# Kernel tuning notes

Hardware: AMD Instinct MI355X
Metric: run time of the kernel (lower is better)

Reference implementation:

```python
import jax, jax.numpy as jnp
import numpy as np
from jax import lax

HEADS = 4
NEG_SLOPE = 0.2


def _layernorm(x, g, b, eps=1e-5):
    m = x.mean(-1, keepdims=True)
    v = ((x - m) ** 2).mean(-1, keepdims=True)
    return (x - m) * lax.rsqrt(v + eps) * g + b


def setup_inputs() -> dict:
    key = jax.random.key(0)
    ks = jax.random.split(key, 10)
    B, N, T, H, E, ED, K = 1, 1000, 32, 128, 16000, 16, 3
    s_h = 1.0 / np.sqrt(H)
    s_e = 1.0 / np.sqrt(ED)
    return {
        "x": jax.random.normal(ks[0], (B, N, T, H), jnp.float32),
        "edge_index": jax.random.randint(ks[1], (2, E), 0, N, dtype=jnp.int32),
        "edge_attr": jax.random.normal(ks[2], (E, ED), jnp.float32),
        "conv_w": jax.random.normal(ks[3], (H, H, K), jnp.float32) * (1.0 / np.sqrt(H * K)),
        "conv_b": jnp.zeros((H,), jnp.float32),
        "ln1_g": jnp.ones((H,), jnp.float32),
        "ln1_b": jnp.zeros((H,), jnp.float32),
        "Wl": jax.random.normal(ks[4], (H, H), jnp.float32) * s_h,
        "Wr": jax.random.normal(ks[5], (H, H), jnp.float32) * s_h,
        "We": jax.random.normal(ks[6], (ED, H), jnp.float32) * s_e,
        "att": jax.random.normal(ks[7], (HEADS, H // HEADS), jnp.float32) * s_h,
        "gat_b": jnp.zeros((H,), jnp.float32),
        "ln2_g": jnp.ones((H,), jnp.float32),
        "ln2_b": jnp.zeros((H,), jnp.float32),
    }


def reference(x, edge_index, edge_attr, conv_w, conv_b, ln1_g, ln1_b,
              Wl, Wr, We, att, gat_b, ln2_g, ln2_b):
    B, N, T, H = x.shape
    K = HEADS
    D = H // K
    E = edge_attr.shape[0]

    # ---- temporal sub-block: per-node Conv1d over time ('same' padding) ----
    xt = x.reshape(B * N, T, H).transpose(0, 2, 1)            # [BN, H, T]
    y = lax.conv_general_dilated(xt, conv_w, (1,), 'SAME',
                                 dimension_numbers=('NCH', 'OIH', 'NCH'))
    y = y + conv_b[None, :, None]
    y = y.transpose(0, 2, 1).reshape(B, N, T, H)
    x = _layernorm(x + y, ln1_g, ln1_b)

    # ---- spatial sub-block: GATv2 at every timestep (mega-batch of G graphs) ----
    G = B * T
    xs = x.transpose(0, 2, 1, 3).reshape(G, N, H)             # [G, N, H]

    # add self-loops, fill_value='mean' (mean of incoming edge attrs per node)
    dst0 = edge_index[1]
    cnt = jax.ops.segment_sum(jnp.ones((E,), edge_attr.dtype), dst0, num_segments=N)
    loop_attr = jax.ops.segment_sum(edge_attr, dst0, num_segments=N) / jnp.maximum(cnt, 1.0)[:, None]
    ea = jnp.concatenate([edge_attr, loop_attr], axis=0)       # [E+N, ED]
    loops = jnp.arange(N, dtype=edge_index.dtype)
    src = jnp.concatenate([edge_index[0], loops])
    dst = jnp.concatenate([edge_index[1], loops])

    gl = jnp.einsum('gnh,hkd->gnkd', xs, Wl.reshape(H, K, D))  # source transform
    gr = jnp.einsum('gnh,hkd->gnkd', xs, Wr.reshape(H, K, D))  # target transform
    ee = jnp.einsum('ef,fkd->ekd', ea, We.reshape(-1, K, D))   # edge transform

    e_src = jnp.swapaxes(gl[:, src], 0, 1)                     # [E', G, K, D]
    e_dst = jnp.swapaxes(gr[:, dst], 0, 1)                     # [E', G, K, D]
    s = jax.nn.leaky_relu(e_src + e_dst + ee[:, None], NEG_SLOPE)
    logits = jnp.einsum('egkd,kd->egk', s, att)                # [E', G, K]

    # scatter-softmax over incoming edges per target node (self-loops => non-empty)
    mx = jax.ops.segment_max(logits, dst, num_segments=N)[dst]
    ex = jnp.exp(logits - mx)
    den = jax.ops.segment_sum(ex, dst, num_segments=N)[dst]
    alpha = ex / den

    aggr = jax.ops.segment_sum(e_src * alpha[..., None], dst, num_segments=N)  # [N, G, K, D]
    out = jnp.swapaxes(aggr, 0, 1).reshape(G, N, H) + gat_b

    out = out.reshape(B, T, N, H).transpose(0, 2, 1, 3)        # back to (B, N, T, H)
    return _layernorm(x + out, ln2_g, ln2_b)
```

## Files before the change

kernel.cpp:

```cpp
#include <hip/hip_runtime.h>
#include <math.h>

#define N_NODES 1000
#define T_STEPS 32
#define H_DIM   128
#define E_EDGES 16000
#define ED_DIM  16
#define G_GRAPHS 32
#define EP_EDGES (E_EDGES + N_NODES)
#define NEG_SLOPE 0.2f
#define LN_EPS 1e-5f

typedef __attribute__((ext_vector_type(8))) short bf16x8;
typedef __attribute__((ext_vector_type(16))) float f32x16;
typedef __attribute__((ext_vector_type(4))) float f32x4;
typedef unsigned short u16;

__device__ inline short f2bf(float f) {
    unsigned u = __float_as_uint(f);
    u = (u + 0x7FFFu + ((u >> 16) & 1u)) >> 16;
    return (short)u;
}
__device__ inline float bf2f(u16 u) { return __uint_as_float(((unsigned)u) << 16); }
__device__ inline float bflo(unsigned u) { return __uint_as_float(u << 16); }
__device__ inline float bfhi(unsigned u) { return __uint_as_float(u & 0xFFFF0000u); }

__global__ void k_pack(const float* __restrict__ conv_w, const float* __restrict__ Wl,
                       const float* __restrict__ Wr, short* __restrict__ wc,
                       short* __restrict__ wg) {
    int i = blockIdx.x * 256 + threadIdx.x;
    if (i < 4 * 24 * 64 * 8) {
        int r = i & 7, lane = (i >> 3) & 63;
        int t = i >> 9;
        int kstep = t % 24, ct = t / 24;
        int k = kstep >> 3, hs = kstep & 7;
        int hi = hs * 16 + ((lane >> 5) << 3) + r;
        int o = ct * 32 + (lane & 31);
        wc[i] = f2bf(conv_w[(o * H_DIM + hi) * 3 + k]);
    } else {
        int j = i - 4 * 24 * 64 * 8;
        if (j >= 8 * 8 * 64 * 8) return;
        int r = j & 7, lane = (j >> 3) & 63;
        int ks = (j >> 9) & 7, ct = j >> 12;
        int hi = ks * 16 + ((lane >> 5) << 3) + r;
        int o = ct * 32 + (lane & 31);
        wg[j] = f2bf(o < H_DIM ? Wl[hi * H_DIM + o] : Wr[hi * H_DIM + o - H_DIM]);
    }
}

__global__ __launch_bounds__(1024) void k_countscan(const int* __restrict__ dst,
                                                    int* __restrict__ cnt, int* __restrict__ cnt2,
                                                    int* __restrict__ offs) {
    __shared__ int sm[1024];
    int t = threadIdx.x;
    sm[t] = 0;
    __syncthreads();
    for (int e = t; e < E_EDGES; e += 1024) atomicAdd(&sm[dst[e]], 1);
    __syncthreads();
    int v = (t < N_NODES) ? sm[t] : 0;
    if (t < N_NODES) { cnt[t] = v; cnt2[t] = 0; }
    __syncthreads();
    sm[t] = v;
    for (int s = 1; s < 1024; s <<= 1) {
        __syncthreads();
        int a = (t >= s) ? sm[t - s] : 0;
        __syncthreads();
        sm[t] += a;
    }
    __syncthreads();
    if (t < N_NODES) offs[t + 1] = sm[t];
    if (t == 0) offs[0] = 0;
}

__global__ void k_place(const int* __restrict__ dst, const int* __restrict__ offs,
                        int* __restrict__ cnt2, int* __restrict__ csr) {
    int e = blockIdx.x * 256 + threadIdx.x;
    if (e >= E_EDGES) return;
    int d = dst[e];
    int slot = atomicAdd(&cnt2[d], 1);
    csr[offs[d] + slot] = e;
}

__global__ __launch_bounds__(64) void k_sortla(
    const float* __restrict__ edge_attr, int* __restrict__ csr,
    const int* __restrict__ offs, const int* __restrict__ cnt,
    float* __restrict__ loop_attr) {
    __shared__ int buf[128];
    int n = blockIdx.x;
    int lane = threadIdx.x;
    int off = offs[n], deg = cnt[n];

    if (deg <= 64) {
        int v = (lane < deg) ? csr[off + lane] : 0x7FFFFFFF;
        int rank = 0;
#pragma unroll
        for (int j = 0; j < 64; ++j) {
            int vj = __shfl(v, j);
            rank += (vj < v) ? 1 : 0;
        }
        if (lane < deg) buf[rank] = v;
    } else {
        for (int i = lane; i < deg && i < 128; i += 64) buf[i] = csr[off + i];
        __syncthreads();
        if (lane == 0) {
            int dd = deg < 128 ? deg : 128;
            for (int i = 1; i < dd; ++i) {
                int key = buf[i], j = i - 1;
                while (j >= 0 && buf[j] > key) { buf[j + 1] = buf[j]; --j; }
                buf[j + 1] = key;
            }
        }
    }
    __syncthreads();
    if (lane < deg) csr[off + lane] = buf[lane];

    int q = lane >> 4, f = lane & 15;
    float a = 0.f;
    for (int i = q; i < deg; i += 4) a += edge_attr[buf[i] * ED_DIM + f];
    a += __shfl_xor(a, 16);
    a += __shfl_xor(a, 32);
    if (lane < 16) loop_attr[n * ED_DIM + lane] = a / fmaxf((float)deg, 1.0f);
}

__global__ void k_ee(const float* __restrict__ edge_attr, const float* __restrict__ loop_attr,
                     const float* __restrict__ We, u16* __restrict__ ee) {
    int e = blockIdx.x * 2 + (threadIdx.x >> 7);
    int h = threadIdx.x & 127;
    if (e >= EP_EDGES) return;
    const float* ea = (e < E_EDGES) ? &edge_attr[e * ED_DIM]
                                    : &loop_attr[(e - E_EDGES) * ED_DIM];
    float acc = 0.f;
#pragma unroll
    for (int f = 0; f < ED_DIM; ++f) acc += ea[f] * We[f * H_DIM + h];
    ee[e * H_DIM + h] = (u16)f2bf(acc);
}

__global__ __launch_bounds__(256) void k_temporal(
    const float* __restrict__ x, const short* __restrict__ wc, const short* __restrict__ wg,
    const float* __restrict__ conv_b, const float* __restrict__ ln1_g,
    const float* __restrict__ ln1_b, float* __restrict__ x1,
    u16* __restrict__ gl, u16* __restrict__ gr) {
    __shared__ __align__(16) short xb[34 * 136];
    __shared__ float yb[32 * 132];
    int n = blockIdx.x;
    int tid = threadIdx.x;
    int w = tid >> 6, lane = tid & 63;
    int arow = lane & 31;
    int aks = (lane >> 5) << 3;

    {
        const float4* xs4 = (const float4*)(x + (size_t)n * T_STEPS * H_DIM);
        for (int i4 = tid; i4 < T_STEPS * H_DIM / 4; i4 += 256) {
            float4 v = xs4[i4];
            int t = i4 >> 5, h = (i4 * 4) & 127;
            uint2 pp;
            pp.x = (unsigned)(unsigned short)f2bf(v.x) | ((unsigned)(unsigned short)f2bf(v.y) << 16);
            pp.y = (unsigned)(unsigned short)f2bf(v.z) | ((unsigned)(unsigned short)f2bf(v.w) << 16);
            *(uint2*)&xb[(t + 1) * 136 + h] = pp;
        }
        if (tid < 68) {
            ((unsigned*)xb)[tid] = 0u;
            ((unsigned*)(xb + 33 * 136))[tid] = 0u;
        }
    }
    __syncthreads();

    f32x16 acc = {};
    for (int kk = 0; kk < 3; ++kk) {
#pragma unroll
        for (int hs = 0; hs < 8; ++hs) {
            int kstep = kk * 8 + hs;
            bf16x8 a = *(const bf16x8*)&xb[(arow + kk) * 136 + hs * 16 + aks];
            bf16x8 b = *(const bf16x8*)&wc[((w * 24 + kstep) * 64 + lane) * 8];
            acc = __builtin_amdgcn_mfma_f32_32x32x16_bf16(a, b, acc, 0, 0, 0);
        }
    }
    {
        int oc = w * 32 + (lane & 31);
        float cb = conv_b[oc];
#pragma unroll
        for (int r = 0; r < 16; ++r) {
            int t = (r & 3) + 8 * (r >> 2) + 4 * (lane >> 5);
            yb[t * 132 + oc] = acc[r] + cb;
        }
    }
    __syncthreads();

    for (int t = w; t < T_STEPS; t += 4) {
        float r0 = x[((size_t)n * T_STEPS + t) * H_DIM + lane] + yb[t * 132 + lane];
        float r1 = x[((size_t)n * T_STEPS + t) * H_DIM + lane + 64] + yb[t * 132 + lane + 64];
        float s = r0 + r1, s2 = r0 * r0 + r1 * r1;
#pragma unroll
        for (int mm = 1; mm < 64; mm <<= 1) {
            s += __shfl_xor(s, mm);
            s2 += __shfl_xor(s2, mm);
        }
        float mean = s * (1.f / 128.f);
        float var = s2 * (1.f / 128.f) - mean * mean;
        float rs = rsqrtf(var + LN_EPS);
        float o0 = (r0 - mean) * rs * ln1_g[lane] + ln1_b[lane];
        float o1 = (r1 - mean) * rs * ln1_g[lane + 64] + ln1_b[lane + 64];
        x1[((size_t)n * T_STEPS + t) * H_DIM + lane] = o0;
        x1[((size_t)n * T_STEPS + t) * H_DIM + lane + 64] = o1;
        xb[t * 136 + lane] = f2bf(o0);
        xb[t * 136 + lane + 64] = f2bf(o1);
    }
    __syncthreads();

    f32x16 cl = {}, cr = {};
#pragma unroll
    for (int ks = 0; ks < 8; ++ks) {
        bf16x8 a = *(const bf16x8*)&xb[arow * 136 + ks * 16 + aks];
        bf16x8 b0 = *(const bf16x8*)&wg[(((2 * w) * 8 + ks) * 64 + lane) * 8];
        bf16x8 b1 = *(const bf16x8*)&wg[(((2 * w + 1) * 8 + ks) * 64 + lane) * 8];
        cl = __builtin_amdgcn_mfma_f32_32x32x16_bf16(a, b0, cl, 0, 0, 0);
        cr = __builtin_amdgcn_mfma_f32_32x32x16_bf16(a, b1, cr, 0, 0, 0);
    }
    {
        int o0 = 64 * w + (lane & 31);
        u16* d = (w < 2) ? gl : gr;
        int oo0 = (w < 2) ? o0 : o0 - 128;
        int oo1 = oo0 + 32;
#pragma unroll
        for (int r = 0; r < 16; ++r) {
            int t = (r & 3) + 8 * (r >> 2) + 4 * (lane >> 5);
            d[((size_t)t * N_NODES + n) * H_DIM + oo0] = (u16)f2bf(cl[r]);
            d[((size_t)t * N_NODES + n) * H_DIM + oo1] = (u16)f2bf(cr[r]);
        }
    }
}

__global__ __launch_bounds__(128) void k_gat(
    const u16* __restrict__ gl, const u16* __restrict__ gr, const u16* __restrict__ ee,
    const int* __restrict__ src_arr, const int* __restrict__ csr,
    const int* __restrict__ offs, const int* __restrict__ cnt,
    const float* __restrict__ att, const float* __restrict__ gat_b,
    const float* __restrict__ x1, const float* __restrict__ ln2_g,
    const float* __restrict__ ln2_b, float* __restrict__ out) {
    int bid = blockIdx.x;
    int q = bid & 3;
    int n = bid >> 2;
    int tid = threadIdx.x;
    int gs = tid >> 4;
    int r = tid & 15;
    int h0 = ((r >> 2) << 5) + ((r & 3) << 3);
    int g = q + 4 * gs;

    __shared__ int es[64], ss[64];
    int off = offs[n], deg = cnt[n];
    int tot = deg + 1;

    float av[8], grv[8];
    {
        float4 a0 = *(const float4*)&att[h0];
        float4 a1 = *(const float4*)&att[h0 + 4];
        av[0] = a0.x; av[1] = a0.y; av[2] = a0.z; av[3] = a0.w;
        av[4] = a1.x; av[5] = a1.y; av[6] = a1.z; av[7] = a1.w;
        uint4 g4 = *(const uint4*)&gr[((size_t)g * N_NODES + n) * H_DIM + h0];
        grv[0] = bflo(g4.x); grv[1] = bfhi(g4.x); grv[2] = bflo(g4.y); grv[3] = bfhi(g4.y);
        grv[4] = bflo(g4.z); grv[5] = bfhi(g4.z); grv[6] = bflo(g4.w); grv[7] = bfhi(g4.w);
    }
    const u16* glg = gl + (size_t)g * N_NODES * H_DIM + h0;
    const u16* eeh = ee + h0;

    float m = -INFINITY, l = 0.f;
    float ac[8] = {0.f, 0.f, 0.f, 0.f, 0.f, 0.f, 0.f, 0.f};

    for (int base = 0; base < tot; base += 64) {
        int c = min(64, tot - base);
        __syncthreads();
        if (tid < c) {
            int i = base + tid;
            int e = (i < deg) ? csr[off + i] : (E_EDGES + n);
            es[tid] = e;
            ss[tid] = (i < deg) ? src_arr[e] : n;
        }
        __syncthreads();
        uint4 gv4 = *(const uint4*)&glg[(size_t)ss[0] * H_DIM];
        uint4 ev4 = *(const uint4*)&eeh[(size_t)es[0] * H_DIM];
        for (int i = 0; i < c; ++i) {
            uint4 gc = gv4, ec = ev4;
            if (i + 1 < c) {
                gv4 = *(const uint4*)&glg[(size_t)ss[i + 1] * H_DIM];
                ev4 = *(const uint4*)&eeh[(size_t)es[i + 1] * H_DIM];
            }
            float gv[8];
            gv[0] = bflo(gc.x); gv[1] = bfhi(gc.x); gv[2] = bflo(gc.y); gv[3] = bfhi(gc.y);
            gv[4] = bflo(gc.z); gv[5] = bfhi(gc.z); gv[6] = bflo(gc.w); gv[7] = bfhi(gc.w);
            float ev[8];
            ev[0] = bflo(ec.x); ev[1] = bfhi(ec.x); ev[2] = bflo(ec.y); ev[3] = bfhi(ec.y);
            ev[4] = bflo(ec.z); ev[5] = bfhi(ec.z); ev[6] = bflo(ec.w); ev[7] = bfhi(ec.w);
            float p = 0.f;
#pragma unroll
            for (int j = 0; j < 8; ++j) {
                float sf = gv[j] + grv[j] + ev[j];
                sf = fmaxf(sf, NEG_SLOPE * sf);
                p = fmaf(sf, av[j], p);
            }
            p += __shfl_xor(p, 1);
            p += __shfl_xor(p, 2);
            bool grow = p > m + 8.f;
            if (__any(grow)) {
                float mn = fmaxf(m, p);
                float sc = __expf(m - mn);
                float wq = __expf(p - mn);
                l = l * sc + wq;
#pragma unroll
                for (int j = 0; j < 8; ++j) ac[j] = ac[j] * sc + wq * gv[j];
                m = mn;
            } else {
                float wq = __expf(p - m);
                l += wq;
#pragma unroll
                for (int j = 0; j < 8; ++j) ac[j] += wq * gv[j];
            }
        }
    }

    float linv = 1.0f / l;
    size_t ob = ((size_t)n * T_STEPS + g) * H_DIM + h0;
    float4 x0 = *(const float4*)&x1[ob];
    float4 x1v = *(const float4*)&x1[ob + 4];
    float4 gb0 = *(const float4*)&gat_b[h0];
    float4 gb1 = *(const float4*)&gat_b[h0 + 4];
    float rv[8];
    rv[0] = x0.x + ac[0] * linv + gb0.x;
    rv[1] = x0.y + ac[1] * linv + gb0.y;
    rv[2] = x0.z + ac[2] * linv + gb0.z;
    rv[3] = x0.w + ac[3] * linv + gb0.w;
    rv[4] = x1v.x + ac[4] * linv + gb1.x;
    rv[5] = x1v.y + ac[5] * linv + gb1.y;
    rv[6] = x1v.z + ac[6] * linv + gb1.z;
    rv[7] = x1v.w + ac[7] * linv + gb1.w;
    float s1 = 0.f, s2v = 0.f;
#pragma unroll
    for (int j = 0; j < 8; ++j) { s1 += rv[j]; s2v += rv[j] * rv[j]; }
#pragma unroll
    for (int mm = 1; mm < 16; mm <<= 1) {
        s1 += __shfl_xor(s1, mm);
        s2v += __shfl_xor(s2v, mm);
    }
    float mean = s1 * (1.f / 128.f);
    float var = s2v * (1.f / 128.f) - mean * mean;
    float rs = rsqrtf(var + LN_EPS);
    float4 g20 = *(const float4*)&ln2_g[h0];
    float4 g21 = *(const float4*)&ln2_g[h0 + 4];
    float4 b20 = *(const float4*)&ln2_b[h0];
    float4 b21 = *(const float4*)&ln2_b[h0 + 4];
    f32x4 o0, o1;
    o0.x = (rv[0] - mean) * rs * g20.x + b20.x;
    o0.y = (rv[1] - mean) * rs * g20.y + b20.y;
    o0.z = (rv[2] - mean) * rs * g20.z + b20.z;
    o0.w = (rv[3] - mean) * rs * g20.w + b20.w;
    o1.x = (rv[4] - mean) * rs * g21.x + b21.x;
    o1.y = (rv[5] - mean) * rs * g21.y + b21.y;
    o1.z = (rv[6] - mean) * rs * g21.z + b21.z;
    o1.w = (rv[7] - mean) * rs * g21.w + b21.w;
    __builtin_nontemporal_store(o0, (f32x4*)&out[ob]);
    __builtin_nontemporal_store(o1, (f32x4*)&out[ob + 4]);
}

extern "C" void kernel_launch(void* const* d_in, const int* in_sizes, int n_in,
                              void* d_out, int out_size, void* d_ws, size_t ws_size,
                              hipStream_t stream) {
    const float* x         = (const float*)d_in[0];
    const int*   ei        = (const int*)d_in[1];
    const float* edge_attr = (const float*)d_in[2];
    const float* conv_w    = (const float*)d_in[3];
    const float* conv_b    = (const float*)d_in[4];
    const float* ln1_g     = (const float*)d_in[5];
    const float* ln1_b     = (const float*)d_in[6];
    const float* Wl        = (const float*)d_in[7];
    const float* Wr        = (const float*)d_in[8];
    const float* We        = (const float*)d_in[9];
    const float* att       = (const float*)d_in[10];
    const float* gat_b     = (const float*)d_in[11];
    const float* ln2_g     = (const float*)d_in[12];
    const float* ln2_b     = (const float*)d_in[13];
    float* out = (float*)d_out;

    const int* src = ei;
    const int* dst = ei + E_EDGES;

    float* x1   = (float*)d_ws;
    u16*   glb  = (u16*)(x1 + 4096000);
    u16*   grb  = glb + 4096000;
    u16*   eeb  = grb + 4096000;
    float* la   = (float*)(eeb + 2176000);
    int* ibase  = (int*)(la + 16000);
    int* cnt    = ibase;
    int* cnt2   = ibase + 1000;
    int* offs   = ibase + 2000;
    int* csr    = ibase + 3001;
    short* wc   = (short*)(ibase + 19008);
    short* wg   = wc + 49152;

    k_pack<<<320, 256, 0, stream>>>(conv_w, Wl, Wr, wc, wg);
    k_countscan<<<1, 1024, 0, stream>>>(dst, cnt, cnt2, offs);
    k_place<<<(E_EDGES + 255) / 256, 256, 0, stream>>>(dst, offs, cnt2, csr);
    k_sortla<<<N_NODES, 64, 0, stream>>>(edge_attr, csr, offs, cnt, la);
    k_ee<<<(EP_EDGES + 1) / 2, 256, 0, stream>>>(edge_attr, la, We, eeb);
    k_temporal<<<N_NODES, 256, 0, stream>>>(x, wc, wg, conv_b, ln1_g, ln1_b, x1, glb, grb);
    k_gat<<<4 * N_NODES, 128, 0, stream>>>(glb, grb, eeb, src, csr, offs, cnt,
                                           att, gat_b, x1, ln2_g, ln2_b, out);
}
```

Baseline: 88.94 us.

## Merge preprocessing kernels and simplify GAT online softmax inner loop

Five small preprocessing launches become two. Weight packing, degree counting, the scan and CSR placement share one launch, and CSR sorting, self-loop attribute means and the edge transform share another. This cuts launch overhead and the serial gaps between tiny kernels. In the GAT kernel, edge-feature loads become nontemporal and the branchy lazy-rescale softmax becomes an unconditional rescale, trading extra exps per edge for less divergence and shorter control flow.

```diff
diff --git a/kernel.cpp b/kernel.cpp
--- a/kernel.cpp
+++ b/kernel.cpp
@@ -14,6 +14,7 @@
 typedef __attribute__((ext_vector_type(8))) short bf16x8;
 typedef __attribute__((ext_vector_type(16))) float f32x16;
 typedef __attribute__((ext_vector_type(4))) float f32x4;
+typedef __attribute__((ext_vector_type(4))) unsigned u32x4;
 typedef unsigned short u16;
 
 __device__ inline short f2bf(float f) {
@@ -21,46 +22,44 @@
     u = (u + 0x7FFFu + ((u >> 16) & 1u)) >> 16;
     return (short)u;
 }
-__device__ inline float bf2f(u16 u) { return __uint_as_float(((unsigned)u) << 16); }
 __device__ inline float bflo(unsigned u) { return __uint_as_float(u << 16); }
 __device__ inline float bfhi(unsigned u) { return __uint_as_float(u & 0xFFFF0000u); }
 
-__global__ void k_pack(const float* __restrict__ conv_w, const float* __restrict__ Wl,
-                       const float* __restrict__ Wr, short* __restrict__ wc,
-                       short* __restrict__ wg) {
-    int i = blockIdx.x * 256 + threadIdx.x;
-    if (i < 4 * 24 * 64 * 8) {
-        int r = i & 7, lane = (i >> 3) & 63;
-        int t = i >> 9;
-        int kstep = t % 24, ct = t / 24;
-        int k = kstep >> 3, hs = kstep & 7;
-        int hi = hs * 16 + ((lane >> 5) << 3) + r;
-        int o = ct * 32 + (lane & 31);
-        wc[i] = f2bf(conv_w[(o * H_DIM + hi) * 3 + k]);
-    } else {
-        int j = i - 4 * 24 * 64 * 8;
-        if (j >= 8 * 8 * 64 * 8) return;
-        int r = j & 7, lane = (j >> 3) & 63;
-        int ks = (j >> 9) & 7, ct = j >> 12;
-        int hi = ks * 16 + ((lane >> 5) << 3) + r;
-        int o = ct * 32 + (lane & 31);
-        wg[j] = f2bf(o < H_DIM ? Wl[hi * H_DIM + o] : Wr[hi * H_DIM + o - H_DIM]);
-    }
-}
-
-__global__ __launch_bounds__(1024) void k_countscan(const int* __restrict__ dst,
-                                                    int* __restrict__ cnt, int* __restrict__ cnt2,
-                                                    int* __restrict__ offs) {
+__global__ __launch_bounds__(1024) void k_prep(
+    const float* __restrict__ conv_w, const float* __restrict__ Wl,
+    const float* __restrict__ Wr, const int* __restrict__ dst,
+    short* __restrict__ wc, short* __restrict__ wg,
+    int* __restrict__ cnt, int* __restrict__ offs, int* __restrict__ csr) {
+    int b = blockIdx.x;
+    if (b < 80) {
+        int i = b * 1024 + threadIdx.x;
+        if (i < 4 * 24 * 64 * 8) {
+            int r = i & 7, lane = (i >> 3) & 63;
+            int t = i >> 9;
+            int kstep = t % 24, ct = t / 24;
+            int k = kstep >> 3, hs = kstep & 7;
+            int hi = hs * 16 + ((lane >> 5) << 3) + r;
+            int o = ct * 32 + (lane & 31);
+            wc[i] = f2bf(conv_w[(o * H_DIM + hi) * 3 + k]);
+        } else {
+            int j = i - 4 * 24 * 64 * 8;
+            int r = j & 7, lane = (j >> 3) & 63;
+            int ks = (j >> 9) & 7, ct = j >> 12;
+            int hi = ks * 16 + ((lane >> 5) << 3) + r;
+            int o = ct * 32 + (lane & 31);
+            wg[j] = f2bf(o < H_DIM ? Wl[hi * H_DIM + o] : Wr[hi * H_DIM + o - H_DIM]);
+        }
+        return;
+    }
     __shared__ int sm[1024];
+    __shared__ int sl[1024];
     int t = threadIdx.x;
     sm[t] = 0;
     __syncthreads();
     for (int e = t; e < E_EDGES; e += 1024) atomicAdd(&sm[dst[e]], 1);
     __syncthreads();
     int v = (t < N_NODES) ? sm[t] : 0;
-    if (t < N_NODES) { cnt[t] = v; cnt2[t] = 0; }
-    __syncthreads();
-    sm[t] = v;
+    if (t < N_NODES) cnt[t] = v;
     for (int s = 1; s < 1024; s <<= 1) {
         __syncthreads();
         int a = (t >= s) ? sm[t - s] : 0;
@@ -70,39 +69,43 @@
     __syncthreads();
     if (t < N_NODES) offs[t + 1] = sm[t];
     if (t == 0) offs[0] = 0;
-}
-
-__global__ void k_place(const int* __restrict__ dst, const int* __restrict__ offs,
-                        int* __restrict__ cnt2, int* __restrict__ csr) {
-    int e = blockIdx.x * 256 + threadIdx.x;
-    if (e >= E_EDGES) return;
-    int d = dst[e];
-    int slot = atomicAdd(&cnt2[d], 1);
-    csr[offs[d] + slot] = e;
-}
-
-__global__ __launch_bounds__(64) void k_sortla(
-    const float* __restrict__ edge_attr, int* __restrict__ csr,
-    const int* __restrict__ offs, const int* __restrict__ cnt,
-    float* __restrict__ loop_attr) {
-    __shared__ int buf[128];
-    int n = blockIdx.x;
-    int lane = threadIdx.x;
-    int off = offs[n], deg = cnt[n];
-
-    if (deg <= 64) {
-        int v = (lane < deg) ? csr[off + lane] : 0x7FFFFFFF;
-        int rank = 0;
-#pragma unroll
-        for (int j = 0; j < 64; ++j) {
-            int vj = __shfl(v, j);
-            rank += (vj < v) ? 1 : 0;
-        }
-        if (lane < deg) buf[rank] = v;
-    } else {
-        for (int i = lane; i < deg && i < 128; i += 64) buf[i] = csr[off + i];
-        __syncthreads();
-        if (lane == 0) {
+    sl[t] = sm[t] - v;
+    __syncthreads();
+    for (int e = t; e < E_EDGES; e += 1024) {
+        int d = dst[e];
+        int s = atomicAdd(&sl[d], 1);
+        csr[s] = e;
+    }
+}
+
+__global__ __launch_bounds__(256) void k_graphprep(
+    const float* __restrict__ edge_attr, const float* __restrict__ We,
+    int* __restrict__ csr, const int* __restrict__ offs, const int* __restrict__ cnt,
+    u16* __restrict__ ee) {
+    int b = blockIdx.x;
+    int tid = threadIdx.x;
+    if (b < N_NODES) {
+        __shared__ int buf[128];
+        __shared__ float laf[16];
+        int n = b;
+        int off = offs[n], deg = cnt[n];
+        bool fast = (deg <= 64);
+        if (fast) {
+            if (tid < 64) {
+                int v = (tid < deg) ? csr[off + tid] : 0x7FFFFFFF;
+                int rank = 0;
+#pragma unroll
+                for (int j = 0; j < 64; ++j) {
+                    int vj = __shfl(v, j);
+                    rank += (vj < v) ? 1 : 0;
+                }
+                if (tid < deg) buf[rank] = v;
+            }
+        } else {
+            for (int i = tid; i < deg && i < 128; i += 256) buf[i] = csr[off + i];
+        }
+        __syncthreads();
+        if (!fast && tid == 0) {
             int dd = deg < 128 ? deg : 128;
             for (int i = 1; i < dd; ++i) {
                 int key = buf[i], j = i - 1;
@@ -110,29 +113,33 @@
                 buf[j + 1] = key;
             }
         }
-    }
-    __syncthreads();
-    if (lane < deg) csr[off + lane] = buf[lane];
-
-    int q = lane >> 4, f = lane & 15;
-    float a = 0.f;
-    for (int i = q; i < deg; i += 4) a += edge_attr[buf[i] * ED_DIM + f];
-    a += __shfl_xor(a, 16);
-    a += __shfl_xor(a, 32);
-    if (lane < 16) loop_attr[n * ED_DIM + lane] = a / fmaxf((float)deg, 1.0f);
-}
-
-__global__ void k_ee(const float* __restrict__ edge_attr, const float* __restrict__ loop_attr,
-                     const float* __restrict__ We, u16* __restrict__ ee) {
-    int e = blockIdx.x * 2 + (threadIdx.x >> 7);
-    int h = threadIdx.x & 127;
-    if (e >= EP_EDGES) return;
-    const float* ea = (e < E_EDGES) ? &edge_attr[e * ED_DIM]
-                                    : &loop_attr[(e - E_EDGES) * ED_DIM];
-    float acc = 0.f;
-#pragma unroll
-    for (int f = 0; f < ED_DIM; ++f) acc += ea[f] * We[f * H_DIM + h];
-    ee[e * H_DIM + h] = (u16)f2bf(acc);
+        __syncthreads();
+        if (tid < deg && tid < 128) csr[off + tid] = buf[tid];
+        if (tid < 64) {
+            int q = tid >> 4, f = tid & 15;
+            float a = 0.f;
+            for (int i = q; i < deg; i += 4) a += edge_attr[buf[i] * ED_DIM + f];
+            a += __shfl_xor(a, 16);
+            a += __shfl_xor(a, 32);
+            if (tid < 16) laf[tid] = a / fmaxf((float)deg, 1.0f);
+        }
+        __syncthreads();
+        if (tid < H_DIM) {
+            float acc = 0.f;
+#pragma unroll
+            for (int f = 0; f < ED_DIM; ++f) acc += laf[f] * We[f * H_DIM + tid];
+            ee[(size_t)(E_EDGES + n) * H_DIM + tid] = (u16)f2bf(acc);
+        }
+    } else {
+        int e = (b - N_NODES) * 2 + (tid >> 7);
+        int h = tid & 127;
+        if (e >= E_EDGES) return;
+        const float* ea = &edge_attr[e * ED_DIM];
+        float acc = 0.f;
+#pragma unroll
+        for (int f = 0; f < ED_DIM; ++f) acc += ea[f] * We[f * H_DIM + h];
+        ee[(size_t)e * H_DIM + h] = (u16)f2bf(acc);
+    }
 }
 
 __global__ __launch_bounds__(256) void k_temporal(
@@ -256,7 +263,7 @@
         float4 a1 = *(const float4*)&att[h0 + 4];
         av[0] = a0.x; av[1] = a0.y; av[2] = a0.z; av[3] = a0.w;
         av[4] = a1.x; av[5] = a1.y; av[6] = a1.z; av[7] = a1.w;
-        uint4 g4 = *(const uint4*)&gr[((size_t)g * N_NODES + n) * H_DIM + h0];
+        u32x4 g4 = *(const u32x4*)&gr[((size_t)g * N_NODES + n) * H_DIM + h0];
         grv[0] = bflo(g4.x); grv[1] = bfhi(g4.x); grv[2] = bflo(g4.y); grv[3] = bfhi(g4.y);
         grv[4] = bflo(g4.z); grv[5] = bfhi(g4.z); grv[6] = bflo(g4.w); grv[7] = bfhi(g4.w);
     }
@@ -276,44 +283,35 @@
             ss[tid] = (i < deg) ? src_arr[e] : n;
         }
         __syncthreads();
-        uint4 gv4 = *(const uint4*)&glg[(size_t)ss[0] * H_DIM];
-        uint4 ev4 = *(const uint4*)&eeh[(size_t)es[0] * H_DIM];
+        u32x4 gv4 = *(const u32x4*)&glg[(size_t)ss[0] * H_DIM];
+        u32x4 ev4 = __builtin_nontemporal_load((const u32x4*)&eeh[(size_t)es[0] * H_DIM]);
         for (int i = 0; i < c; ++i) {
-            uint4 gc = gv4, ec = ev4;
+            u32x4 gc = gv4, ec = ev4;
             if (i + 1 < c) {
-                gv4 = *(const uint4*)&glg[(size_t)ss[i + 1] * H_DIM];
-                ev4 = *(const uint4*)&eeh[(size_t)es[i + 1] * H_DIM];
+                gv4 = *(const u32x4*)&glg[(size_t)ss[i + 1] * H_DIM];
+                ev4 = __builtin_nontemporal_load((const u32x4*)&eeh[(size_t)es[i + 1] * H_DIM]);
             }
             float gv[8];
             gv[0] = bflo(gc.x); gv[1] = bfhi(gc.x); gv[2] = bflo(gc.y); gv[3] = bfhi(gc.y);
             gv[4] = bflo(gc.z); gv[5] = bfhi(gc.z); gv[6] = bflo(gc.w); gv[7] = bfhi(gc.w);
-            float ev[8];
-            ev[0] = bflo(ec.x); ev[1] = bfhi(ec.x); ev[2] = bflo(ec.y); ev[3] = bfhi(ec.y);
-            ev[4] = bflo(ec.z); ev[5] = bfhi(ec.z); ev[6] = bflo(ec.w); ev[7] = bfhi(ec.w);
             float p = 0.f;
 #pragma unroll
             for (int j = 0; j < 8; ++j) {
-                float sf = gv[j] + grv[j] + ev[j];
+                float evj = (j & 1) ? bfhi(((const unsigned*)&ec)[j >> 1])
+                                    : bflo(((const unsigned*)&ec)[j >> 1]);
+                float sf = gv[j] + grv[j] + evj;
                 sf = fmaxf(sf, NEG_SLOPE * sf);
                 p = fmaf(sf, av[j], p);
             }
             p += __shfl_xor(p, 1);
             p += __shfl_xor(p, 2);
-            bool grow = p > m + 8.f;
-            if (__any(grow)) {
-                float mn = fmaxf(m, p);
-                float sc = __expf(m - mn);
-                float wq = __expf(p - mn);
-                l = l * sc + wq;
-#pragma unroll
-                for (int j = 0; j < 8; ++j) ac[j] = ac[j] * sc + wq * gv[j];
-                m = mn;
-            } else {
-                float wq = __expf(p - m);
-                l += wq;
-#pragma unroll
-                for (int j = 0; j < 8; ++j) ac[j] += wq * gv[j];
-            }
+            float mn = fmaxf(m, p);
+            float sc = __expf(m - mn);
+            float wq = __expf(p - mn);
+            l = l * sc + wq;
+#pragma unroll
+            for (int j = 0; j < 8; ++j) ac[j] = ac[j] * sc + wq * gv[j];
+            m = mn;
         }
     }
 
@@ -395,11 +393,9 @@
     short* wc   = (short*)(ibase + 19008);
     short* wg   = wc + 49152;
 
-    k_pack<<<320, 256, 0, stream>>>(conv_w, Wl, Wr, wc, wg);
-    k_countscan<<<1, 1024, 0, stream>>>(dst, cnt, cnt2, offs);
-    k_place<<<(E_EDGES + 255) / 256, 256, 0, stream>>>(dst, offs, cnt2, csr);
-    k_sortla<<<N_NODES, 64, 0, stream>>>(edge_attr, csr, offs, cnt, la);
-    k_ee<<<(EP_EDGES + 1) / 2, 256, 0, stream>>>(edge_attr, la, We, eeb);
+    k_prep<<<81, 1024, 0, stream>>>(conv_w, Wl, Wr, dst, wc, wg, cnt, offs, csr);
+    k_graphprep<<<N_NODES + (E_EDGES + 1) / 2, 256, 0, stream>>>(edge_attr, We, csr, offs,
+                                                                 cnt, eeb);
     k_temporal<<<N_NODES, 256, 0, stream>>>(x, wc, wg, conv_b, ln1_g, ln1_b, x1, glb, grb);
     k_gat<<<4 * N_NODES, 128, 0, stream>>>(glb, grb, eeb, src, csr, offs, cnt,
                                            att, gat_b, x1, ln2_g, ln2_b, out);
```

Result: faster. 84.57 us (-4.9%).
